# Kernel tuning notes

Measured on AMD Instinct MI355X. Metric: run time of the kernel, lower is better.

The kernel has to match this reference:

```python
import jax, jax.numpy as jnp
import numpy as np

N = 50000
E = 400000
DIM_IN = 512
DIM_H = 64
HEADS = 8
DIM_OUT = 40
SLOPE = 0.2  # PyG GATv2Conv default negative_slope


def setup_inputs() -> dict:
    key = jax.random.key(0)
    ks = jax.random.split(key, 16)
    s = 0.05
    return {
        "x": jax.random.normal(ks[0], (N, DIM_IN), dtype=jnp.float32),
        "edge_index": jax.random.randint(ks[1], (2, E), 0, N, dtype=jnp.int64),
        "Wl1": jax.random.normal(ks[2], (DIM_IN, HEADS * DIM_H), dtype=jnp.float32) * s,
        "Wr1": jax.random.normal(ks[3], (DIM_IN, HEADS * DIM_H), dtype=jnp.float32) * s,
        "att1": jax.random.normal(ks[4], (HEADS, DIM_H), dtype=jnp.float32) * s,
        "b1": jax.random.normal(ks[5], (HEADS * DIM_H,), dtype=jnp.float32) * s,
        "Wl2": jax.random.normal(ks[6], (HEADS * DIM_H, DIM_OUT), dtype=jnp.float32) * s,
        "Wr2": jax.random.normal(ks[7], (HEADS * DIM_H, DIM_OUT), dtype=jnp.float32) * s,
        "att2": jax.random.normal(ks[8], (1, DIM_OUT), dtype=jnp.float32) * s,
        "b2": jax.random.normal(ks[9], (DIM_OUT,), dtype=jnp.float32) * s,
        "Wl3": jax.random.normal(ks[10], (HEADS * DIM_H, 2), dtype=jnp.float32) * s,
        "Wr3": jax.random.normal(ks[11], (HEADS * DIM_H, 2), dtype=jnp.float32) * s,
        "att3": jax.random.normal(ks[12], (1, 2), dtype=jnp.float32) * s,
        "b3": jax.random.normal(ks[13], (2,), dtype=jnp.float32) * s,
    }


def gatv2(x, src, dst, Wl, Wr, att, b):
    # PyG GATv2Conv: e_ij = att . LeakyReLU(W_l x_j + W_r x_i); softmax over j (by dst i);
    # out_i = sum_j alpha_ij * (W_l x_j); heads concatenated; bias added after.
    n = x.shape[0]
    H, F = att.shape
    xl = (x @ Wl).reshape(n, H, F)  # source transform
    xr = (x @ Wr).reshape(n, H, F)  # target transform
    e = jax.nn.leaky_relu(xl[src] + xr[dst], negative_slope=SLOPE)  # [E, H, F]
    logits = jnp.einsum("ehf,hf->eh", e, att)  # [E, H]
    m = jax.ops.segment_max(logits, dst, num_segments=n)  # self-loops => every segment nonempty
    ex = jnp.exp(logits - m[dst])
    denom = jax.ops.segment_sum(ex, dst, num_segments=n)
    alpha = ex / denom[dst]  # [E, H]
    out = jax.ops.segment_sum(xl[src] * alpha[:, :, None], dst, num_segments=n)  # [N, H, F]
    return out.reshape(n, H * F) + b


def reference(x, edge_index, Wl1, Wr1, att1, b1, Wl2, Wr2, att2, b2, Wl3, Wr3, att3, b3):
    # add self loops (PyG default add_self_loops=True)
    loops = jnp.arange(N, dtype=edge_index.dtype)
    ei = jnp.concatenate([edge_index, jnp.stack([loops, loops])], axis=1)
    src, dst = ei[0], ei[1]
    # eval mode: dropout is identity; ReverseLayerF is identity in forward
    h = jax.nn.relu(gatv2(x, src, dst, Wl1, Wr1, att1, b1))
    y_class = gatv2(h, src, dst, Wl2, Wr2, att2, b2)
    y_domain = gatv2(h, src, dst, Wl3, Wr3, att3, b3)
    return (y_class, y_domain)
```

## Files before the change

kernel.cpp:

```cpp
#include <hip/hip_runtime.h>
#include <math.h>

typedef unsigned short u16;
typedef unsigned int   u32;
typedef __attribute__((ext_vector_type(8))) short bf16x8;
typedef __attribute__((ext_vector_type(4))) float f32x4;
typedef __attribute__((ext_vector_type(4))) u32   u32x4;

__device__ __forceinline__ float b2f(u16 u) {
  union { u32 i; float f; } v; v.i = ((u32)u) << 16; return v.f;
}
__device__ __forceinline__ u16 f2b(float f) {
  union { u32 i; float f; } v; v.f = f;
  u32 r = v.i + 0x7FFFu + ((v.i >> 16) & 1u);
  return (u16)(r >> 16);
}
__device__ __forceinline__ float blo(u32 w) {
  union { u32 i; float f; } v; v.i = w << 16; return v.f;
}
__device__ __forceinline__ float bhi(u32 w) {
  union { u32 i; float f; } v; v.i = w & 0xFFFF0000u; return v.f;
}
__device__ __forceinline__ void ld_lds16(const u16* g, u16* l) {
  __builtin_amdgcn_global_load_lds((const __attribute__((address_space(1))) void*)g,
                                   (__attribute__((address_space(3))) void*)l, 16, 0, 0);
}

#define NN 50000
#define NE 400000
#define NT 450000
#define NBLK_SCAN 196

__global__ void k_detect(const void* x, const void* ei, int* flags) {
  __shared__ int cnt[2];
  int t = threadIdx.x;
  if (t < 2) cnt[t] = 0;
  __syncthreads();
  u16 u = ((const u16*)x)[t];
  int e = (u >> 7) & 0xFF;
  if (u == 0 || (e >= 90 && e <= 134)) atomicAdd(&cnt[0], 1);
  if (t < 16) {
    if (((const int*)ei)[2 * t + 1] == 0) atomicAdd(&cnt[1], 1);
  }
  __syncthreads();
  if (t == 0) {
    flags[0] = (cnt[0] >= 110) ? 1 : 0;
    flags[1] = (cnt[1] >= 15) ? 1 : 0;
  }
}

__device__ __forceinline__ int eidx(const int* ei, int pos, int i64) {
  return i64 ? ei[2 * pos] : ei[pos];
}

__global__ void k_convert_x(const void* x, const int* flags, u16* xb) {
  if (flags[0]) return;
  int c = blockIdx.x * 256 + threadIdx.x;
  const float* xf = (const float*)x + (size_t)c * 8;
  u32x4 o;
  #pragma unroll
  for (int i = 0; i < 4; ++i) {
    u32 lo = f2b(xf[2 * i]);
    u32 hi = f2b(xf[2 * i + 1]);
    o[i] = lo | (hi << 16);
  }
  *(u32x4*)(xb + (size_t)c * 8) = o;
}

__global__ void k_pack_w1t(const void* Wl1, const void* Wr1, const int* flags, u16* w1t) {
  int t = blockIdx.x * 256 + threadIdx.x;
  int k = t >> 10;
  int c = t & 1023;
  const void* W = (c < 512) ? Wl1 : Wr1;
  int cc = c & 511;
  u16 v;
  if (flags[0]) v = ((const u16*)W)[k * 512 + cc];
  else          v = f2b(((const float*)W)[k * 512 + cc]);
  w1t[c * 512 + k] = v;
}

__global__ void k_pack_w23t(const void* Wl2, const void* Wr2, const void* Wl3, const void* Wr3,
                            const int* flags, u16* w23t) {
  int t = blockIdx.x * 256 + threadIdx.x;
  int k = t / 96;
  int c = t % 96;
  const void* W = nullptr; int idx = 0;
  if (c < 40)      { W = Wl2; idx = k * 40 + c; }
  else if (c < 42) { W = Wl3; idx = k * 2 + (c - 40); }
  else if (c < 82) { W = Wr2; idx = k * 40 + (c - 42); }
  else if (c < 84) { W = Wr3; idx = k * 2 + (c - 82); }
  u16 v = 0;
  if (W) {
    if (flags[0]) v = ((const u16*)W)[idx];
    else          v = f2b(((const float*)W)[idx]);
  }
  w23t[c * 512 + k] = v;
}

__global__ void k_pack_params(const void* att1, const void* b1, const void* att2, const void* b2,
                              const void* att3, const void* b3, const int* flags, float* params) {
  int t = blockIdx.x * 256 + threadIdx.x;
  if (t >= 1108) return;
  const void* src; int idx;
  if (t < 512)       { src = att1; idx = t; }
  else if (t < 1024) { src = b1;   idx = t - 512; }
  else if (t < 1064) { src = att2; idx = t - 1024; }
  else if (t < 1104) { src = b2;   idx = t - 1064; }
  else if (t < 1106) { src = att3; idx = t - 1104; }
  else               { src = b3;   idx = t - 1106; }
  params[t] = flags[0] ? b2f(((const u16*)src)[idx]) : ((const float*)src)[idx];
}

__global__ void k_hist(const int* ei, const int* flags, int* deg) {
  int e = blockIdx.x * 256 + threadIdx.x;
  if (e >= NE) return;
  int d = eidx(ei, NE + e, flags[1]);
  atomicAdd(&deg[d], 1);
}

__global__ void k_scanA(const int* deg, int* row_ptr, int* bsum) {
  __shared__ int sh[256];
  int b = blockIdx.x, t = threadIdx.x;
  int i = b * 256 + t;
  int val = (i < NN) ? deg[i] + 1 : 0;
  sh[t] = val;
  __syncthreads();
  #pragma unroll
  for (int off = 1; off < 256; off <<= 1) {
    int v = (t >= off) ? sh[t - off] : 0;
    __syncthreads();
    sh[t] += v;
    __syncthreads();
  }
  if (i < NN) row_ptr[i] = sh[t] - val;
  if (t == 255) bsum[b] = sh[255];
}

__global__ void k_scanB(int* bsum, int* row_ptr) {
  __shared__ int sh[256];
  int t = threadIdx.x;
  int val = (t < NBLK_SCAN) ? bsum[t] : 0;
  sh[t] = val;
  __syncthreads();
  #pragma unroll
  for (int off = 1; off < 256; off <<= 1) {
    int v = (t >= off) ? sh[t - off] : 0;
    __syncthreads();
    sh[t] += v;
    __syncthreads();
  }
  if (t < NBLK_SCAN) bsum[t] = sh[t] - val;
  if (t == 255) row_ptr[NN] = sh[255];
}

__global__ void k_scanC(const int* bsum, int* row_ptr, int* cursor) {
  int i = blockIdx.x * 256 + threadIdx.x;
  if (i < NN) {
    int v = row_ptr[i] + bsum[blockIdx.x];
    row_ptr[i] = v;
    cursor[i] = v;
  }
}

__global__ void k_scatter(const int* ei, const int* flags, int* cursor, int* csr_src) {
  int t = blockIdx.x * 256 + threadIdx.x;
  if (t >= NT) return;
  int i64 = flags[1];
  int s, d;
  if (t < NE) { s = eidx(ei, t, i64); d = eidx(ei, NE + t, i64); }
  else        { s = d = t - NE; }
  int pos = atomicAdd(&cursor[d], 1);
  csr_src[pos] = s;
}

__global__ __launch_bounds__(256) void k_gemm1(const void* __restrict__ xraw, const u16* __restrict__ xb,
                                               const u16* __restrict__ Bt, const int* __restrict__ flags,
                                               const float* __restrict__ params,
                                               u16* __restrict__ XL, u16* __restrict__ XR,
                                               float* __restrict__ dotL, float* __restrict__ dotR) {
  __shared__ __align__(16) u16 As[128 * 64];
  __shared__ __align__(16) u16 Bs[128 * 64];
  const int id  = blockIdx.x;
  const int xcd = id & 7;
  const int lb  = id >> 3;
  const int mt  = xcd * 49 + (lb >> 3);
  const int nt  = lb & 7;
  if (mt >= 391) return;
  const int m0 = mt * 128;
  const int n0 = nt * 128;
  const u16* __restrict__ A = flags[0] ? (const u16*)xraw : xb;
  const int t = threadIdx.x;
  const int wave = t >> 6;
  const int lane = t & 63;
  const int wm = (wave >> 1) * 64;
  const int wn = (wave & 1) * 64;
  const int fr = lane & 15;
  const int fk = lane >> 4;
  const int srow = lane >> 3;
  const int schk = (lane & 7) ^ srow;
  f32x4 acc[4][4] = {};
  for (int k0 = 0; k0 < 512; k0 += 64) {
    #pragma unroll
    for (int q = 0; q < 4; ++q) {
      int rbase = wave * 32 + q * 8;
      int gm = m0 + rbase + srow;
      if (gm > NN - 1) gm = NN - 1;
      ld_lds16(&A[(size_t)gm * 512 + k0 + schk * 8], &As[rbase * 64]);
      ld_lds16(&Bt[(size_t)(n0 + rbase + srow) * 512 + k0 + schk * 8], &Bs[rbase * 64]);
    }
    __syncthreads();
    #pragma unroll
    for (int h = 0; h < 2; ++h) {
      int s = h * 4 + fk;
      bf16x8 af[4], bb[4];
      #pragma unroll
      for (int i = 0; i < 4; ++i) {
        int row = wm + i * 16 + fr;
        af[i] = *(const bf16x8*)&As[row * 64 + ((s ^ (row & 7)) * 8)];
      }
      #pragma unroll
      for (int j = 0; j < 4; ++j) {
        int row = wn + j * 16 + fr;
        bb[j] = *(const bf16x8*)&Bs[row * 64 + ((s ^ (row & 7)) * 8)];
      }
      #pragma unroll
      for (int i = 0; i < 4; ++i)
        #pragma unroll
        for (int j = 0; j < 4; ++j)
          acc[i][j] = __builtin_amdgcn_mfma_f32_16x16x32_bf16(af[i], bb[j], acc[i][j], 0, 0, 0);
    }
    __syncthreads();
  }
  {
    const int cb = (n0 + wn) & 511;
    const bool isL = (n0 + wn) < 512;
    const int hd = cb >> 6;
    float* __restrict__ dvec = isL ? dotL : dotR;
    float attv[4];
    #pragma unroll
    for (int j = 0; j < 4; ++j) attv[j] = params[cb + j * 16 + fr];
    #pragma unroll
    for (int i = 0; i < 4; ++i) {
      #pragma unroll
      for (int r = 0; r < 4; ++r) {
        float d = attv[0] * acc[i][0][r];
        d = fmaf(attv[1], acc[i][1][r], d);
        d = fmaf(attv[2], acc[i][2][r], d);
        d = fmaf(attv[3], acc[i][3][r], d);
        d += __shfl_xor(d, 1, 64);
        d += __shfl_xor(d, 2, 64);
        d += __shfl_xor(d, 4, 64);
        d += __shfl_xor(d, 8, 64);
        int gm = m0 + wm + i * 16 + fk * 4 + r;
        if (fr == 0 && gm < NN) dvec[(size_t)gm * 8 + hd] = 0.6f * d;
      }
    }
  }
  #pragma unroll
  for (int i = 0; i < 4; ++i) {
    #pragma unroll
    for (int r = 0; r < 4; ++r) {
      int gm = m0 + wm + i * 16 + fk * 4 + r;
      if (gm < NN) {
        #pragma unroll
        for (int j = 0; j < 4; ++j) {
          int gn = n0 + wn + j * 16 + fr;
          u16 v = f2b(acc[i][j][r]);
          if (gn < 512) XL[(size_t)gm * 512 + gn] = v;
          else          XR[(size_t)gm * 512 + gn - 512] = v;
        }
      }
    }
  }
}

__global__ __launch_bounds__(256) void k_gemm2(const u16* __restrict__ A, const u16* __restrict__ Bt,
                                               float* __restrict__ C) {
  __shared__ __align__(16) short As[128][40];
  __shared__ __align__(16) short Bs[96][40];
  const int m0 = blockIdx.x * 128;
  const int t = threadIdx.x;
  const int wave = t >> 6;
  const int lane = t & 63;
  const int fr = lane & 15;
  const int fk = lane >> 4;
  const int wm = wave * 32;
  f32x4 acc[2][6] = {};
  for (int k0 = 0; k0 < 512; k0 += 32) {
    #pragma unroll
    for (int h = 0; h < 2; ++h) {
      int c = t + h * 256;
      int row = c >> 2, kc = (c & 3) * 8;
      int gm = m0 + row;
      u32x4 va = {0, 0, 0, 0};
      if (gm < NN) va = *(const u32x4*)&A[(size_t)gm * 512 + k0 + kc];
      *(u32x4*)&As[row][kc] = va;
    }
    for (int c = t; c < 384; c += 256) {
      int row = c >> 2, kc = (c & 3) * 8;
      *(u32x4*)&Bs[row][kc] = *(const u32x4*)&Bt[row * 512 + k0 + kc];
    }
    __syncthreads();
    bf16x8 af[2], bb[6];
    #pragma unroll
    for (int i = 0; i < 2; ++i) af[i] = *(const bf16x8*)&As[wm + i * 16 + fr][fk * 8];
    #pragma unroll
    for (int j = 0; j < 6; ++j) bb[j] = *(const bf16x8*)&Bs[j * 16 + fr][fk * 8];
    #pragma unroll
    for (int i = 0; i < 2; ++i)
      #pragma unroll
      for (int j = 0; j < 6; ++j)
        acc[i][j] = __builtin_amdgcn_mfma_f32_16x16x32_bf16(af[i], bb[j], acc[i][j], 0, 0, 0);
    __syncthreads();
  }
  #pragma unroll
  for (int i = 0; i < 2; ++i) {
    #pragma unroll
    for (int j = 0; j < 6; ++j) {
      int gn = j * 16 + fr;
      if (gn < 84) {
        #pragma unroll
        for (int r = 0; r < 4; ++r) {
          int gm = m0 + wm + i * 16 + fk * 4 + r;
          if (gm < NN) C[(size_t)gm * 84 + gn] = acc[i][j][r];
        }
      }
    }
  }
}

__global__ __launch_bounds__(256) void k_layer1f(const u16* __restrict__ xl1, const u16* __restrict__ xr1,
                                                 const float* __restrict__ dotL, const float* __restrict__ dotR,
                                                 const int* __restrict__ row_ptr, const int* __restrict__ csr_src,
                                                 const float* __restrict__ params, u16* __restrict__ hb) {
  int wid = blockIdx.x * 4 + (threadIdx.x >> 6);
  int lane = threadIdx.x & 63;
  int nw = gridDim.x * 4;
  int grp = lane >> 3;
  float att[8];
  #pragma unroll
  for (int k = 0; k < 8; ++k) att[k] = 0.4f * params[lane * 8 + k];
  for (int i = wid; i < NN; i += nw) {
    int e0 = row_ptr[i], e1 = row_ptr[i + 1];
    u32x4 xrv = *(const u32x4*)&xr1[(size_t)i * 512 + lane * 8];
    float dRi = dotR[(size_t)i * 8 + grp];
    float xr[8];
    #pragma unroll
    for (int q = 0; q < 4; ++q) { xr[2 * q] = blo(xrv[q]); xr[2 * q + 1] = bhi(xrv[q]); }
    float s = 0.f;
    float acc[8] = {0.f, 0.f, 0.f, 0.f, 0.f, 0.f, 0.f, 0.f};
    int q0 = csr_src[e0];
    int q1 = csr_src[e0 + 1 < e1 ? e0 + 1 : e1 - 1];
    int q2 = csr_src[e0 + 2 < e1 ? e0 + 2 : e1 - 1];
    int q3 = csr_src[e0 + 3 < e1 ? e0 + 3 : e1 - 1];
    for (int p = e0; p < e1; p += 4) {
      int j0 = q0, j1 = q1, j2 = q2, j3 = q3;
      u32x4 v0 = *(const u32x4*)&xl1[(size_t)j0 * 512 + lane * 8];
      u32x4 v1 = *(const u32x4*)&xl1[(size_t)j1 * 512 + lane * 8];
      u32x4 v2 = *(const u32x4*)&xl1[(size_t)j2 * 512 + lane * 8];
      u32x4 v3 = *(const u32x4*)&xl1[(size_t)j3 * 512 + lane * 8];
      float dl0 = dotL[(size_t)j0 * 8 + grp];
      float dl1 = dotL[(size_t)j1 * 8 + grp];
      float dl2 = dotL[(size_t)j2 * 8 + grp];
      float dl3 = dotL[(size_t)j3 * 8 + grp];
      int np = p + 4;
      if (np < e1) {
        q0 = csr_src[np];
        q1 = csr_src[np + 1 < e1 ? np + 1 : e1 - 1];
        q2 = csr_src[np + 2 < e1 ? np + 2 : e1 - 1];
        q3 = csr_src[np + 3 < e1 ? np + 3 : e1 - 1];
      }
      float m1 = (p + 1 < e1) ? 1.f : 0.f;
      float m2 = (p + 2 < e1) ? 1.f : 0.f;
      float m3 = (p + 3 < e1) ? 1.f : 0.f;
      float c0 = 0.f, c1 = 0.f, c2 = 0.f, c3 = 0.f;
      float xlv0[8], xlv1[8], xlv2[8], xlv3[8];
      #pragma unroll
      for (int q = 0; q < 4; ++q) {
        xlv0[2 * q] = blo(v0[q]); xlv0[2 * q + 1] = bhi(v0[q]);
        xlv1[2 * q] = blo(v1[q]); xlv1[2 * q + 1] = bhi(v1[q]);
        xlv2[2 * q] = blo(v2[q]); xlv2[2 * q + 1] = bhi(v2[q]);
        xlv3[2 * q] = blo(v3[q]); xlv3[2 * q + 1] = bhi(v3[q]);
      }
      #pragma unroll
      for (int k = 0; k < 8; ++k) {
        float t0 = xlv0[k] + xr[k];
        float t1 = xlv1[k] + xr[k];
        float t2 = xlv2[k] + xr[k];
        float t3 = xlv3[k] + xr[k];
        c0 = fmaf(att[k], fabsf(t0), c0);
        c1 = fmaf(att[k], fabsf(t1), c1);
        c2 = fmaf(att[k], fabsf(t2), c2);
        c3 = fmaf(att[k], fabsf(t3), c3);
      }
      c0 += __shfl_xor(c0, 1, 64); c1 += __shfl_xor(c1, 1, 64);
      c2 += __shfl_xor(c2, 1, 64); c3 += __shfl_xor(c3, 1, 64);
      c0 += __shfl_xor(c0, 2, 64); c1 += __shfl_xor(c1, 2, 64);
      c2 += __shfl_xor(c2, 2, 64); c3 += __shfl_xor(c3, 2, 64);
      c0 += __shfl_xor(c0, 4, 64); c1 += __shfl_xor(c1, 4, 64);
      c2 += __shfl_xor(c2, 4, 64); c3 += __shfl_xor(c3, 4, 64);
      float l0 = c0 + dl0 + dRi;
      float l1 = c1 + dl1 + dRi;
      float l2 = c2 + dl2 + dRi;
      float l3 = c3 + dl3 + dRi;
      float pv0 = __expf(fminf(fmaxf(l0, -30.f), 30.f));
      float pv1 = __expf(fminf(fmaxf(l1, -30.f), 30.f)) * m1;
      float pv2 = __expf(fminf(fmaxf(l2, -30.f), 30.f)) * m2;
      float pv3 = __expf(fminf(fmaxf(l3, -30.f), 30.f)) * m3;
      s += (pv0 + pv1) + (pv2 + pv3);
      #pragma unroll
      for (int k = 0; k < 8; ++k) {
        float a = fmaf(pv0, xlv0[k], acc[k]);
        a = fmaf(pv1, xlv1[k], a);
        a = fmaf(pv2, xlv2[k], a);
        acc[k] = fmaf(pv3, xlv3[k], a);
      }
    }
    float r = 1.f / s;
    u32x4 o;
    #pragma unroll
    for (int q = 0; q < 4; ++q) {
      u32 lo = f2b(fmaxf(fmaf(acc[2 * q],     r, params[512 + lane * 8 + 2 * q]),     0.f));
      u32 hi = f2b(fmaxf(fmaf(acc[2 * q + 1], r, params[512 + lane * 8 + 2 * q + 1]), 0.f));
      o[q] = lo | (hi << 16);
    }
    *(u32x4*)&hb[(size_t)i * 512 + lane * 8] = o;
  }
}

__global__ __launch_bounds__(256) void k_layer23f(const float* __restrict__ xlr23, const int* __restrict__ row_ptr,
                                                  const int* __restrict__ csr_src, const float* __restrict__ params,
                                                  const int* __restrict__ flags, void* __restrict__ out) {
  int wid = blockIdx.x * 4 + (threadIdx.x >> 6);
  int lane = threadIdx.x & 63;
  int nw = gridDim.x * 4;
  int c = lane;
  bool act = c < 42;
  float att = 0.f;
  if (c < 40)      att = params[1024 + c];
  else if (c < 42) att = params[1104 + (c - 40)];
  int isbf = flags[0];
  for (int i = wid; i < NN; i += nw) {
    int e0 = row_ptr[i], e1 = row_ptr[i + 1];
    float xr = act ? xlr23[(size_t)i * 84 + 42 + c] : 0.f;
    float s2 = 0.f, s3 = 0.f, acc = 0.f;
    for (int p = e0; p < e1; p += 2) {
      int p1 = p + 1 < e1 ? p + 1 : e1 - 1;
      float m1 = (p + 1 < e1) ? 1.f : 0.f;
      int j0 = csr_src[p], j1 = csr_src[p1];
      float xl0 = act ? xlr23[(size_t)j0 * 84 + c] : 0.f;
      float xl1 = act ? xlr23[(size_t)j1 * 84 + c] : 0.f;
      float t0 = xl0 + xr, t1 = xl1 + xr;
      float v0 = att * fmaxf(t0, 0.2f * t0);
      float v1 = att * fmaxf(t1, 0.2f * t1);
      float w0 = (c < 40) ? v0 : 0.f;
      float w1 = (c < 40) ? v1 : 0.f;
      #pragma unroll
      for (int o = 32; o >= 1; o >>= 1) { w0 += __shfl_xor(w0, o, 64); w1 += __shfl_xor(w1, o, 64); }
      float u0 = v0 + __shfl_xor(v0, 1, 64);
      float u1 = v1 + __shfl_xor(v1, 1, 64);
      float l3_0 = __shfl(u0, 40, 64);
      float l3_1 = __shfl(u1, 40, 64);
      float p2_0 = __expf(fminf(fmaxf(w0, -30.f), 30.f));
      float p2_1 = __expf(fminf(fmaxf(w1, -30.f), 30.f)) * m1;
      float p3_0 = __expf(fminf(fmaxf(l3_0, -30.f), 30.f));
      float p3_1 = __expf(fminf(fmaxf(l3_1, -30.f), 30.f)) * m1;
      s2 += p2_0 + p2_1;
      s3 += p3_0 + p3_1;
      float a0 = (c < 40) ? p2_0 : p3_0;
      float a1 = (c < 40) ? p2_1 : p3_1;
      acc = fmaf(a1, xl1, fmaf(a0, xl0, acc));
    }
    if (c < 40) {
      float v = acc / s2 + params[1064 + c];
      size_t o = (size_t)i * 40 + c;
      if (isbf) ((u16*)out)[o] = f2b(v); else ((float*)out)[o] = v;
    } else if (c < 42) {
      float v = acc / s3 + params[1106 + (c - 40)];
      size_t o = 2000000 + (size_t)i * 2 + (c - 40);
      if (isbf) ((u16*)out)[o] = f2b(v); else ((float*)out)[o] = v;
    }
  }
}

extern "C" void kernel_launch(void* const* d_in, const int* in_sizes, int n_in,
                              void* d_out, int out_size, void* d_ws, size_t ws_size,
                              hipStream_t stream) {
  const void* x    = d_in[0];
  const int*  ei   = (const int*)d_in[1];
  const void* Wl1  = d_in[2];
  const void* Wr1  = d_in[3];
  const void* att1 = d_in[4];
  const void* b1   = d_in[5];
  const void* Wl2  = d_in[6];
  const void* Wr2  = d_in[7];
  const void* att2 = d_in[8];
  const void* b2   = d_in[9];
  const void* Wl3  = d_in[10];
  const void* Wr3  = d_in[11];
  const void* att3 = d_in[12];
  const void* b3   = d_in[13];
  (void)in_sizes; (void)n_in; (void)out_size;

  char* ws = (char*)d_ws;
  size_t off = 0;
  auto alloc = [&](size_t bytes) -> void* {
    void* p = ws + off;
    off = (off + bytes + 255) & ~(size_t)255;
    return p;
  };
  int*   flags   = (int*)  alloc(64);
  u16*   xb      = (u16*)  alloc((size_t)NN * 512 * 2);
  u16*   w1t     = (u16*)  alloc((size_t)1024 * 512 * 2);
  u16*   xl1     = (u16*)  alloc((size_t)NN * 512 * 2);
  u16*   xr1     = (u16*)  alloc((size_t)NN * 512 * 2);
  u16*   hb      = (u16*)  alloc((size_t)NN * 512 * 2);
  u16*   w23t    = (u16*)  alloc((size_t)96 * 512 * 2);
  float* xlr23   = (float*)alloc((size_t)NN * 84 * 4);
  float* params  = (float*)alloc(1108 * 4);
  float* dotL    = (float*)alloc((size_t)NN * 8 * 4);
  float* dotR    = (float*)alloc((size_t)NN * 8 * 4);
  int*   row_ptr = (int*)  alloc((NN + 1) * 4);
  int*   deg     = (int*)  alloc(NN * 4);
  int*   cursor  = (int*)  alloc(NN * 4);
  int*   csr_src = (int*)  alloc((NT + 16) * 4);
  int*   bsum    = (int*)  alloc(256 * 4);
  if (ws_size < off) return;

  hipLaunchKernelGGL(k_detect, dim3(1), dim3(128), 0, stream, x, (const void*)ei, flags);
  hipLaunchKernelGGL(k_convert_x, dim3(12500), dim3(256), 0, stream, x, flags, xb);
  hipLaunchKernelGGL(k_pack_w1t, dim3(2048), dim3(256), 0, stream, Wl1, Wr1, flags, w1t);
  hipLaunchKernelGGL(k_pack_w23t, dim3(192), dim3(256), 0, stream, Wl2, Wr2, Wl3, Wr3, flags, w23t);
  hipLaunchKernelGGL(k_pack_params, dim3(5), dim3(256), 0, stream, att1, b1, att2, b2, att3, b3, flags, params);
  hipMemsetAsync(deg, 0, NN * 4, stream);
  hipLaunchKernelGGL(k_hist, dim3((NE + 255) / 256), dim3(256), 0, stream, ei, flags, deg);
  hipLaunchKernelGGL(k_scanA, dim3(NBLK_SCAN), dim3(256), 0, stream, deg, row_ptr, bsum);
  hipLaunchKernelGGL(k_scanB, dim3(1), dim3(256), 0, stream, bsum, row_ptr);
  hipLaunchKernelGGL(k_scanC, dim3(NBLK_SCAN), dim3(256), 0, stream, bsum, row_ptr, cursor);
  hipLaunchKernelGGL(k_scatter, dim3((NT + 255) / 256), dim3(256), 0, stream, ei, flags, cursor, csr_src);
  hipLaunchKernelGGL(k_gemm1, dim3(3136), dim3(256), 0, stream, x, xb, w1t, flags, params, xl1, xr1, dotL, dotR);
  hipLaunchKernelGGL(k_layer1f, dim3(4096), dim3(256), 0, stream, xl1, xr1, dotL, dotR, row_ptr, csr_src, params, hb);
  hipLaunchKernelGGL(k_gemm2, dim3(391), dim3(256), 0, stream, hb, w23t, xlr23);
  hipLaunchKernelGGL(k_layer23f, dim3(4096), dim3(256), 0, stream, xlr23, row_ptr, csr_src, params, flags, d_out);
}
```

Baseline: 507.2 us.

## Fold attention dot products into GEMM1 as extra precomputed weight columns

Precomputes W·att vectors for the per-head attention dot terms and appends them as 16 extra columns of the packed layer-1 weight matrix, computed by a new small kernel. GEMM1 gains a ninth column tile that produces the dot terms directly via MFMA, replacing the fp32 epilogue reduction over the bf16-free accumulators with shuffles. This adds a mostly-empty 128-wide tile per row block (only 16 columns used) and slightly changes numerics, since the dots now come from bf16-rounded folded weights.

```diff
diff --git a/kernel.cpp b/kernel.cpp
--- a/kernel.cpp
+++ b/kernel.cpp
@@ -69,14 +69,34 @@
 
 __global__ void k_pack_w1t(const void* Wl1, const void* Wr1, const int* flags, u16* w1t) {
   int t = blockIdx.x * 256 + threadIdx.x;
-  int k = t >> 10;
-  int c = t & 1023;
-  const void* W = (c < 512) ? Wl1 : Wr1;
-  int cc = c & 511;
-  u16 v;
-  if (flags[0]) v = ((const u16*)W)[k * 512 + cc];
-  else          v = f2b(((const float*)W)[k * 512 + cc]);
-  w1t[c * 512 + k] = v;
+  int r = t >> 9;
+  int k = t & 511;
+  u16 v = 0;
+  if (r < 1024) {
+    const void* W = (r < 512) ? Wl1 : Wr1;
+    int cc = r & 511;
+    if (flags[0]) v = ((const u16*)W)[k * 512 + cc];
+    else          v = f2b(((const float*)W)[k * 512 + cc]);
+  }
+  w1t[(size_t)r * 512 + k] = v;
+}
+
+__global__ void k_dotw(const void* Wl1, const void* Wr1, const int* flags,
+                       const float* params, u16* w1t) {
+  int t = blockIdx.x * 256 + threadIdx.x;
+  int k = t >> 4;
+  int c = t & 15;
+  int h = c & 7;
+  const void* W = (c < 8) ? Wl1 : Wr1;
+  int isbf = flags[0];
+  float s = 0.f;
+  #pragma unroll 8
+  for (int f = 0; f < 64; ++f) {
+    float wv = isbf ? b2f(((const u16*)W)[k * 512 + h * 64 + f])
+                    : ((const float*)W)[k * 512 + h * 64 + f];
+    s = fmaf(wv, params[h * 64 + f], s);
+  }
+  w1t[(size_t)(1024 + c) * 512 + k] = f2b(0.6f * s);
 }
 
 __global__ void k_pack_w23t(const void* Wl2, const void* Wr2, const void* Wl3, const void* Wr3,
@@ -175,16 +195,15 @@
 
 __global__ __launch_bounds__(256) void k_gemm1(const void* __restrict__ xraw, const u16* __restrict__ xb,
                                                const u16* __restrict__ Bt, const int* __restrict__ flags,
-                                               const float* __restrict__ params,
                                                u16* __restrict__ XL, u16* __restrict__ XR,
-                                               float* __restrict__ dotL, float* __restrict__ dotR) {
+                                               float* __restrict__ dots) {
   __shared__ __align__(16) u16 As[128 * 64];
   __shared__ __align__(16) u16 Bs[128 * 64];
   const int id  = blockIdx.x;
   const int xcd = id & 7;
   const int lb  = id >> 3;
-  const int mt  = xcd * 49 + (lb >> 3);
-  const int nt  = lb & 7;
+  const int mt  = xcd * 49 + lb / 9;
+  const int nt  = lb % 9;
   if (mt >= 391) return;
   const int m0 = mt * 128;
   const int n0 = nt * 128;
@@ -198,6 +217,7 @@
   const int fk = lane >> 4;
   const int srow = lane >> 3;
   const int schk = (lane & 7) ^ srow;
+  const bool isdot = (nt == 8);
   f32x4 acc[4][4] = {};
   for (int k0 = 0; k0 < 512; k0 += 64) {
     #pragma unroll
@@ -209,52 +229,60 @@
       ld_lds16(&Bt[(size_t)(n0 + rbase + srow) * 512 + k0 + schk * 8], &Bs[rbase * 64]);
     }
     __syncthreads();
-    #pragma unroll
-    for (int h = 0; h < 2; ++h) {
-      int s = h * 4 + fk;
-      bf16x8 af[4], bb[4];
+    if (isdot) {
+      #pragma unroll
+      for (int h = 0; h < 2; ++h) {
+        int s = h * 4 + fk;
+        bf16x8 af[4], b0;
+        #pragma unroll
+        for (int i = 0; i < 4; ++i) {
+          int row = wm + i * 16 + fr;
+          af[i] = *(const bf16x8*)&As[row * 64 + ((s ^ (row & 7)) * 8)];
+        }
+        {
+          int row = wn + fr;
+          b0 = *(const bf16x8*)&Bs[row * 64 + ((s ^ (row & 7)) * 8)];
+        }
+        #pragma unroll
+        for (int i = 0; i < 4; ++i)
+          acc[i][0] = __builtin_amdgcn_mfma_f32_16x16x32_bf16(af[i], b0, acc[i][0], 0, 0, 0);
+      }
+    } else {
+      #pragma unroll
+      for (int h = 0; h < 2; ++h) {
+        int s = h * 4 + fk;
+        bf16x8 af[4], bb[4];
+        #pragma unroll
+        for (int i = 0; i < 4; ++i) {
+          int row = wm + i * 16 + fr;
+          af[i] = *(const bf16x8*)&As[row * 64 + ((s ^ (row & 7)) * 8)];
+        }
+        #pragma unroll
+        for (int j = 0; j < 4; ++j) {
+          int row = wn + j * 16 + fr;
+          bb[j] = *(const bf16x8*)&Bs[row * 64 + ((s ^ (row & 7)) * 8)];
+        }
+        #pragma unroll
+        for (int i = 0; i < 4; ++i)
+          #pragma unroll
+          for (int j = 0; j < 4; ++j)
+            acc[i][j] = __builtin_amdgcn_mfma_f32_16x16x32_bf16(af[i], bb[j], acc[i][j], 0, 0, 0);
+      }
+    }
+    __syncthreads();
+  }
+  if (isdot) {
+    if (wn == 0) {
       #pragma unroll
       for (int i = 0; i < 4; ++i) {
-        int row = wm + i * 16 + fr;
-        af[i] = *(const bf16x8*)&As[row * 64 + ((s ^ (row & 7)) * 8)];
-      }
-      #pragma unroll
-      for (int j = 0; j < 4; ++j) {
-        int row = wn + j * 16 + fr;
-        bb[j] = *(const bf16x8*)&Bs[row * 64 + ((s ^ (row & 7)) * 8)];
-      }
-      #pragma unroll
-      for (int i = 0; i < 4; ++i)
-        #pragma unroll
-        for (int j = 0; j < 4; ++j)
-          acc[i][j] = __builtin_amdgcn_mfma_f32_16x16x32_bf16(af[i], bb[j], acc[i][j], 0, 0, 0);
-    }
-    __syncthreads();
-  }
-  {
-    const int cb = (n0 + wn) & 511;
-    const bool isL = (n0 + wn) < 512;
-    const int hd = cb >> 6;
-    float* __restrict__ dvec = isL ? dotL : dotR;
-    float attv[4];
-    #pragma unroll
-    for (int j = 0; j < 4; ++j) attv[j] = params[cb + j * 16 + fr];
-    #pragma unroll
-    for (int i = 0; i < 4; ++i) {
-      #pragma unroll
-      for (int r = 0; r < 4; ++r) {
-        float d = attv[0] * acc[i][0][r];
-        d = fmaf(attv[1], acc[i][1][r], d);
-        d = fmaf(attv[2], acc[i][2][r], d);
-        d = fmaf(attv[3], acc[i][3][r], d);
-        d += __shfl_xor(d, 1, 64);
-        d += __shfl_xor(d, 2, 64);
-        d += __shfl_xor(d, 4, 64);
-        d += __shfl_xor(d, 8, 64);
-        int gm = m0 + wm + i * 16 + fk * 4 + r;
-        if (fr == 0 && gm < NN) dvec[(size_t)gm * 8 + hd] = 0.6f * d;
-      }
-    }
+        #pragma unroll
+        for (int r = 0; r < 4; ++r) {
+          int gm = m0 + wm + i * 16 + fk * 4 + r;
+          if (gm < NN) dots[(size_t)gm * 16 + fr] = acc[i][0][r];
+        }
+      }
+    }
+    return;
   }
   #pragma unroll
   for (int i = 0; i < 4; ++i) {
@@ -330,7 +358,7 @@
 }
 
 __global__ __launch_bounds__(256) void k_layer1f(const u16* __restrict__ xl1, const u16* __restrict__ xr1,
-                                                 const float* __restrict__ dotL, const float* __restrict__ dotR,
+                                                 const float* __restrict__ dots,
                                                  const int* __restrict__ row_ptr, const int* __restrict__ csr_src,
                                                  const float* __restrict__ params, u16* __restrict__ hb) {
   int wid = blockIdx.x * 4 + (threadIdx.x >> 6);
@@ -343,7 +371,7 @@
   for (int i = wid; i < NN; i += nw) {
     int e0 = row_ptr[i], e1 = row_ptr[i + 1];
     u32x4 xrv = *(const u32x4*)&xr1[(size_t)i * 512 + lane * 8];
-    float dRi = dotR[(size_t)i * 8 + grp];
+    float dRi = dots[(size_t)i * 16 + 8 + grp];
     float xr[8];
     #pragma unroll
     for (int q = 0; q < 4; ++q) { xr[2 * q] = blo(xrv[q]); xr[2 * q + 1] = bhi(xrv[q]); }
@@ -359,10 +387,10 @@
       u32x4 v1 = *(const u32x4*)&xl1[(size_t)j1 * 512 + lane * 8];
       u32x4 v2 = *(const u32x4*)&xl1[(size_t)j2 * 512 + lane * 8];
       u32x4 v3 = *(const u32x4*)&xl1[(size_t)j3 * 512 + lane * 8];
-      float dl0 = dotL[(size_t)j0 * 8 + grp];
-      float dl1 = dotL[(size_t)j1 * 8 + grp];
-      float dl2 = dotL[(size_t)j2 * 8 + grp];
-      float dl3 = dotL[(size_t)j3 * 8 + grp];
+      float dl0 = dots[(size_t)j0 * 16 + grp];
+      float dl1 = dots[(size_t)j1 * 16 + grp];
+      float dl2 = dots[(size_t)j2 * 16 + grp];
+      float dl3 = dots[(size_t)j3 * 16 + grp];
       int np = p + 4;
       if (np < e1) {
         q0 = csr_src[np];
@@ -511,15 +539,14 @@
   };
   int*   flags   = (int*)  alloc(64);
   u16*   xb      = (u16*)  alloc((size_t)NN * 512 * 2);
-  u16*   w1t     = (u16*)  alloc((size_t)1024 * 512 * 2);
+  u16*   w1t     = (u16*)  alloc((size_t)1152 * 512 * 2);
   u16*   xl1     = (u16*)  alloc((size_t)NN * 512 * 2);
   u16*   xr1     = (u16*)  alloc((size_t)NN * 512 * 2);
   u16*   hb      = (u16*)  alloc((size_t)NN * 512 * 2);
   u16*   w23t    = (u16*)  alloc((size_t)96 * 512 * 2);
   float* xlr23   = (float*)alloc((size_t)NN * 84 * 4);
   float* params  = (float*)alloc(1108 * 4);
-  float* dotL    = (float*)alloc((size_t)NN * 8 * 4);
-  float* dotR    = (float*)alloc((size_t)NN * 8 * 4);
+  float* dots    = (float*)alloc((size_t)NN * 16 * 4);
   int*   row_ptr = (int*)  alloc((NN + 1) * 4);
   int*   deg     = (int*)  alloc(NN * 4);
   int*   cursor  = (int*)  alloc(NN * 4);
@@ -529,17 +556,18 @@
 
   hipLaunchKernelGGL(k_detect, dim3(1), dim3(128), 0, stream, x, (const void*)ei, flags);
   hipLaunchKernelGGL(k_convert_x, dim3(12500), dim3(256), 0, stream, x, flags, xb);
-  hipLaunchKernelGGL(k_pack_w1t, dim3(2048), dim3(256), 0, stream, Wl1, Wr1, flags, w1t);
+  hipLaunchKernelGGL(k_pack_w1t, dim3(2304), dim3(256), 0, stream, Wl1, Wr1, flags, w1t);
   hipLaunchKernelGGL(k_pack_w23t, dim3(192), dim3(256), 0, stream, Wl2, Wr2, Wl3, Wr3, flags, w23t);
   hipLaunchKernelGGL(k_pack_params, dim3(5), dim3(256), 0, stream, att1, b1, att2, b2, att3, b3, flags, params);
+  hipLaunchKernelGGL(k_dotw, dim3(32), dim3(256), 0, stream, Wl1, Wr1, flags, params, w1t);
   hipMemsetAsync(deg, 0, NN * 4, stream);
   hipLaunchKernelGGL(k_hist, dim3((NE + 255) / 256), dim3(256), 0, stream, ei, flags, deg);
   hipLaunchKernelGGL(k_scanA, dim3(NBLK_SCAN), dim3(256), 0, stream, deg, row_ptr, bsum);
   hipLaunchKernelGGL(k_scanB, dim3(1), dim3(256), 0, stream, bsum, row_ptr);
   hipLaunchKernelGGL(k_scanC, dim3(NBLK_SCAN), dim3(256), 0, stream, bsum, row_ptr, cursor);
   hipLaunchKernelGGL(k_scatter, dim3((NT + 255) / 256), dim3(256), 0, stream, ei, flags, cursor, csr_src);
-  hipLaunchKernelGGL(k_gemm1, dim3(3136), dim3(256), 0, stream, x, xb, w1t, flags, params, xl1, xr1, dotL, dotR);
-  hipLaunchKernelGGL(k_layer1f, dim3(4096), dim3(256), 0, stream, xl1, xr1, dotL, dotR, row_ptr, csr_src, params, hb);
+  hipLaunchKernelGGL(k_gemm1, dim3(3528), dim3(256), 0, stream, x, xb, w1t, flags, xl1, xr1, dots);
+  hipLaunchKernelGGL(k_layer1f, dim3(4096), dim3(256), 0, stream, xl1, xr1, dots, row_ptr, csr_src, params, hb);
   hipLaunchKernelGGL(k_gemm2, dim3(391), dim3(256), 0, stream, hb, w23t, xlr23);
   hipLaunchKernelGGL(k_layer23f, dim3(4096), dim3(256), 0, stream, xlr23, row_ptr, csr_src, params, flags, d_out);
 }
```

Result: no change. 510.3 us (+0.6%).
